# Optimization experiments

Hardware: AMD Instinct MI355X
Metric: run time of the kernel (lower is better)

The kernel has to match this reference:

```python
import jax, jax.numpy as jnp
import numpy as np

C = 0.11512925464970229  # ln(10)/20
K = 15
FD = 128
FS = 160
OV = 40
MAX_LAG = 256
PAD_L = K // 2
PAD_R = K - 1 - PAD_L
LOG_GAIN_LIMIT = 10 * C
GAIN_A = (6.0 * C - (-6.0 * C)) / 2
GAIN_B = (6.0 * C + (-6.0 * C)) / 2


def setup_inputs() -> dict:
    key = jax.random.key(0)
    ks = jax.random.split(key, 8)
    B, NF = 32, 500
    N = NF * FS
    x = jax.random.normal(ks[0], (B, 1, N), dtype=jnp.float32)
    features = jax.random.normal(ks[1], (B, NF, FD), dtype=jnp.float32)
    lags = jax.random.randint(ks[2], (B, NF), 0, 256)
    s = 1.0 / np.sqrt(FD)
    ck_w = jax.random.normal(ks[3], (K, FD), dtype=jnp.float32) * s
    ck_b = jax.random.normal(ks[4], (K,), dtype=jnp.float32) * 0.01
    fg_w = jax.random.normal(ks[5], (1, FD), dtype=jnp.float32) * s
    fg_b = jnp.full((1,), max(0.1, 4.0 + LOG_GAIN_LIMIT), dtype=jnp.float32)
    gg_w = jax.random.normal(ks[6], (1, FD), dtype=jnp.float32) * s
    gg_b = jax.random.normal(ks[7], (1,), dtype=jnp.float32) * 0.01
    return {"x": x, "features": features, "lags": lags,
            "ck_w": ck_w, "ck_b": ck_b, "fg_w": fg_w, "fg_b": fg_b,
            "gg_w": gg_w, "gg_b": gg_b}


def reference(x, features, lags, ck_w, ck_b, fg_w, fg_b, gg_w, gg_b):
    B, _, N = x.shape
    NF = features.shape[1]
    OUT = FS + OV  # per-frame output length before crossfade

    # per-frame FIR kernels, p=2 normalized over taps
    kernels = jnp.einsum('bfd,kd->bfk', features, ck_w) + ck_b          # (B,NF,K)
    kernels = kernels / (1e-6 + jnp.sqrt(jnp.sum(kernels**2, -1, keepdims=True)))
    # per-frame scalar gains
    gains = jnp.exp(-jax.nn.relu(features @ fg_w[0] + fg_b[0]) + LOG_GAIN_LIMIT)   # (B,NF)
    ggains = jnp.exp(GAIN_A * jnp.tanh(features @ gg_w[0] + gg_b[0]) + GAIN_B)     # (B,NF)

    # pad: [PAD_L,PAD_R] for conv, then [MAX_LAG, OV] for lag gather / final frame
    xp = jnp.pad(x[:, 0, :], ((0, 0), (MAX_LAG + PAD_L, PAD_R + OV)))   # (B,Np)

    L = FS + K - 1 + OV
    t = jnp.arange(L)
    f_off = jnp.arange(NF) * FS
    cidx = t[None, None, :] + f_off[None, :, None] + MAX_LAG - lags[:, :, None]  # (B,NF,L)
    xx = xp[jnp.arange(B)[:, None, None], cidx]                         # (B,NF,L)

    # grouped conv1d == cross-correlation with per-frame kernel
    win = jnp.stack([xx[:, :, k:k + OUT] for k in range(K)], axis=-1)   # (B,NF,OUT,K)
    conv = jnp.einsum('bflk,bfk->bfl', win, kernels)                    # (B,NF,OUT)

    # dry path
    offset = MAX_LAG + PAD_L
    pt_idx = offset + f_off[:, None] + jnp.arange(OUT)[None, :]         # (NF,OUT)
    pt = xp[:, pt_idx]                                                  # (B,NF,OUT)

    new_chunk = ggains[:, :, None] * (conv * gains[:, :, None] + pt)    # (B,NF,OUT)

    # overlap-add crossfade between consecutive frames
    win2 = 0.5 + 0.5 * jnp.cos((jnp.arange(OV) + 0.5) * jnp.pi / OV)
    win1 = win2[::-1]
    tails = new_chunk[:, :, FS:]                                        # (B,NF,OV)
    prev = jnp.concatenate([jnp.zeros_like(tails[:, :1]), tails[:, :-1]], axis=1)
    head = new_chunk[:, :, :OV] * win1 + prev * win2
    out = jnp.concatenate([head, new_chunk[:, :, OV:FS]], axis=-1)      # (B,NF,FS)
    return out.reshape(B, 1, NF * FS)
```

## Files before the change

kernel.cpp:

```cpp
#include <hip/hip_runtime.h>
#include <math.h>

namespace {
constexpr int K = 15;
constexpr int FD = 128;
constexpr int FS = 160;
constexpr int OV = 40;
constexpr int NFRAMES = 500;
constexpr int NSAMP = NFRAMES * FS;
constexpr float C_CONST = 0.11512925464970229f;
constexpr float LOG_GAIN_LIMIT = 10.0f * C_CONST;
constexpr float GAIN_A = 6.0f * C_CONST;
constexpr int FPB = 10;
constexpr int NFR = FPB + 1;
constexpr int WIN = FS + OV + K - 1;
constexpr int SFSTR = 132;
constexpr float PI_F = 3.14159265358979323846f;
}

__global__ __launch_bounds__(256)
void comb_fused(const float* __restrict__ x,
                const float* __restrict__ feat,
                const int*   __restrict__ lags,
                const float* __restrict__ ck_w,
                const float* __restrict__ ck_b,
                const float* __restrict__ fg_w,
                const float* __restrict__ fg_b,
                const float* __restrict__ gg_w,
                const float* __restrict__ gg_b,
                float* __restrict__ out)
{
    const int tid = threadIdx.x;
    const int bid = blockIdx.x;
    const int b   = bid / (NFRAMES / FPB);
    const int blk = bid - b * (NFRAMES / FPB);
    const int f0  = blk * FPB;

    __shared__ float sf[NFR][SFSTR];
    __shared__ float swin[NFR][WIN];
    __shared__ float sdots[NFR][17];
    __shared__ float sfk[NFR][16];
    __shared__ int   sbase[NFR];
    __shared__ int   svalid[NFR];

    const float* xb = x + (size_t)b * NSAMP;

    if (tid < NFR) {
        const int pf = f0 - 1 + tid;
        const int valid = (pf >= 0) ? 1 : 0;
        svalid[tid] = valid;
        sbase[tid]  = valid ? (pf * FS - lags[b * NFRAMES + pf] - 7) : 0;
    }
    for (int i = tid; i < NFR * (FD / 4); i += 256) {
        const int fr = i >> 5;
        const int e4 = i & 31;
        const int pf = f0 - 1 + fr;
        float4 v = make_float4(0.f, 0.f, 0.f, 0.f);
        if (pf >= 0)
            v = ((const float4*)feat)[((size_t)b * NFRAMES + pf) * (FD / 4) + e4];
        *(float4*)&sf[fr][e4 * 4] = v;
    }
    __syncthreads();

    for (int i = tid; i < NFR * WIN; i += 256) {
        const int fr = i / WIN;
        const int l  = i - fr * WIN;
        const int idx = sbase[fr] + l;
        float v = 0.f;
        if (svalid[fr] && idx >= 0 && idx < NSAMP) v = xb[idx];
        swin[fr][l] = v;
    }

    if (tid < NFR * 17) {
        const int fr = tid / 17;
        const int j  = tid - fr * 17;
        const float* wrow = (j < K) ? (ck_w + (size_t)j * FD)
                                    : ((j == K) ? fg_w : gg_w);
        const float4* w4 = (const float4*)wrow;
        const float4* f4 = (const float4*)&sf[fr][0];
        float4 acc = make_float4(0.f, 0.f, 0.f, 0.f);
        #pragma unroll
        for (int i = 0; i < FD / 4; ++i) {
            const float4 a = f4[i];
            const float4 w = w4[i];
            acc.x += a.x * w.x; acc.y += a.y * w.y;
            acc.z += a.z * w.z; acc.w += a.w * w.w;
        }
        const float bias = (j < K) ? ck_b[j] : ((j == K) ? fg_b[0] : gg_b[0]);
        sdots[fr][j] = acc.x + acc.y + acc.z + acc.w + bias;
    }
    __syncthreads();

    if (tid < NFR) {
        const int fr = tid;
        if (!svalid[fr]) {
            #pragma unroll
            for (int k = 0; k < 16; ++k) sfk[fr][k] = 0.f;
        } else {
            float kern[K];
            float n2 = 0.f;
            #pragma unroll
            for (int k = 0; k < K; ++k) {
                kern[k] = sdots[fr][k];
                n2 += kern[k] * kern[k];
            }
            const float inv   = 1.f / (1e-6f + sqrtf(n2));
            const float gain  = expf(-fmaxf(sdots[fr][K], 0.f) + LOG_GAIN_LIMIT);
            const float ggain = expf(GAIN_A * tanhf(sdots[fr][K + 1]));
            const float ks    = ggain * gain * inv;
            #pragma unroll
            for (int k = 0; k < K; ++k) sfk[fr][k] = ks * kern[k];
            sfk[fr][15] = ggain;
        }
    }
    __syncthreads();

    const int obase = f0 * FS;
    for (int o = tid; o < FPB * FS; o += 256) {
        const int frl = o / FS;
        const int t   = o - frl * FS;
        const int fr  = frl + 1;
        const float pt = xb[obase + o];
        float c = 0.f;
        #pragma unroll
        for (int k = 0; k < K; ++k)
            c += swin[fr][t + k] * sfk[fr][k];
        float val = c + sfk[fr][15] * pt;
        if (t < OV) {
            float ct = 0.f;
            #pragma unroll
            for (int k = 0; k < K; ++k)
                ct += swin[fr - 1][FS + t + k] * sfk[fr - 1][k];
            const float tail = ct + sfk[fr - 1][15] * pt;
            const float w2 = 0.5f + 0.5f * cosf(((float)t + 0.5f) * (PI_F / OV));
            val = val * (1.f - w2) + tail * w2;
        }
        out[(size_t)b * NSAMP + obase + o] = val;
    }
}

extern "C" void kernel_launch(void* const* d_in, const int* in_sizes, int n_in,
                              void* d_out, int out_size, void* d_ws, size_t ws_size,
                              hipStream_t stream) {
    const float* x    = (const float*)d_in[0];
    const float* feat = (const float*)d_in[1];
    const int*   lags = (const int*)d_in[2];
    const float* ck_w = (const float*)d_in[3];
    const float* ck_b = (const float*)d_in[4];
    const float* fg_w = (const float*)d_in[5];
    const float* fg_b = (const float*)d_in[6];
    const float* gg_w = (const float*)d_in[7];
    const float* gg_b = (const float*)d_in[8];
    float* out = (float*)d_out;

    const int B = in_sizes[0] / NSAMP;
    const int nblocks = B * (NFRAMES / FPB);
    comb_fused<<<dim3(nblocks), dim3(256), 0, stream>>>(
        x, feat, lags, ck_w, ck_b, fg_w, fg_b, gg_w, gg_b, out);
}
```

Measured before the change: 108.0 us.

## Vectorize window loads and compute four outputs per thread with register reuse

```diff
diff --git a/kernel.cpp b/kernel.cpp
--- a/kernel.cpp
+++ b/kernel.cpp
@@ -13,7 +13,8 @@
 constexpr float GAIN_A = 6.0f * C_CONST;
 constexpr int FPB = 10;
 constexpr int NFR = FPB + 1;
-constexpr int WIN = FS + OV + K - 1;
+constexpr int NW4 = 55;
+constexpr int WINA = 220;
 constexpr int SFSTR = 132;
 constexpr float PI_F = 3.14159265358979323846f;
 }
@@ -36,21 +37,14 @@
     const int blk = bid - b * (NFRAMES / FPB);
     const int f0  = blk * FPB;
 
-    __shared__ float sf[NFR][SFSTR];
-    __shared__ float swin[NFR][WIN];
+    __shared__ __align__(16) float sf[NFR][SFSTR];
+    __shared__ __align__(16) float swin[NFR][WINA];
     __shared__ float sdots[NFR][17];
-    __shared__ float sfk[NFR][16];
-    __shared__ int   sbase[NFR];
-    __shared__ int   svalid[NFR];
+    __shared__ __align__(16) float sfk[NFR][16];
+    __shared__ __align__(16) float swin2[OV + 8];
 
     const float* xb = x + (size_t)b * NSAMP;
 
-    if (tid < NFR) {
-        const int pf = f0 - 1 + tid;
-        const int valid = (pf >= 0) ? 1 : 0;
-        svalid[tid] = valid;
-        sbase[tid]  = valid ? (pf * FS - lags[b * NFRAMES + pf] - 7) : 0;
-    }
     for (int i = tid; i < NFR * (FD / 4); i += 256) {
         const int fr = i >> 5;
         const int e4 = i & 31;
@@ -60,16 +54,30 @@
             v = ((const float4*)feat)[((size_t)b * NFRAMES + pf) * (FD / 4) + e4];
         *(float4*)&sf[fr][e4 * 4] = v;
     }
+
+    for (int i = tid; i < NFR * NW4; i += 256) {
+        const int fr = i / NW4;
+        const int m  = i - fr * NW4;
+        const int pf = f0 - 1 + fr;
+        float4 v = make_float4(0.f, 0.f, 0.f, 0.f);
+        if (pf >= 0) {
+            const int base = pf * FS - lags[b * NFRAMES + pf] - 7;
+            const int idx  = base + 4 * m;
+            if (idx >= 0 && idx + 3 < NSAMP) {
+                v = *(const float4*)(xb + idx);
+            } else {
+                if (idx     >= 0 && idx     < NSAMP) v.x = xb[idx];
+                if (idx + 1 >= 0 && idx + 1 < NSAMP) v.y = xb[idx + 1];
+                if (idx + 2 >= 0 && idx + 2 < NSAMP) v.z = xb[idx + 2];
+                if (idx + 3 >= 0 && idx + 3 < NSAMP) v.w = xb[idx + 3];
+            }
+        }
+        *(float4*)&swin[fr][4 * m] = v;
+    }
+
+    if (tid < OV)
+        swin2[tid] = 0.5f + 0.5f * cosf(((float)tid + 0.5f) * (PI_F / OV));
     __syncthreads();
-
-    for (int i = tid; i < NFR * WIN; i += 256) {
-        const int fr = i / WIN;
-        const int l  = i - fr * WIN;
-        const int idx = sbase[fr] + l;
-        float v = 0.f;
-        if (svalid[fr] && idx >= 0 && idx < NSAMP) v = xb[idx];
-        swin[fr][l] = v;
-    }
 
     if (tid < NFR * 17) {
         const int fr = tid / 17;
@@ -92,50 +100,98 @@
     __syncthreads();
 
     if (tid < NFR) {
-        const int fr = tid;
-        if (!svalid[fr]) {
-            #pragma unroll
-            for (int k = 0; k < 16; ++k) sfk[fr][k] = 0.f;
+        const int pf = f0 - 1 + tid;
+        if (pf < 0) {
+            #pragma unroll
+            for (int k = 0; k < 16; ++k) sfk[tid][k] = 0.f;
         } else {
             float kern[K];
             float n2 = 0.f;
             #pragma unroll
             for (int k = 0; k < K; ++k) {
-                kern[k] = sdots[fr][k];
+                kern[k] = sdots[tid][k];
                 n2 += kern[k] * kern[k];
             }
             const float inv   = 1.f / (1e-6f + sqrtf(n2));
-            const float gain  = expf(-fmaxf(sdots[fr][K], 0.f) + LOG_GAIN_LIMIT);
-            const float ggain = expf(GAIN_A * tanhf(sdots[fr][K + 1]));
+            const float gain  = expf(-fmaxf(sdots[tid][K], 0.f) + LOG_GAIN_LIMIT);
+            const float ggain = expf(GAIN_A * tanhf(sdots[tid][K + 1]));
             const float ks    = ggain * gain * inv;
             #pragma unroll
-            for (int k = 0; k < K; ++k) sfk[fr][k] = ks * kern[k];
-            sfk[fr][15] = ggain;
+            for (int k = 0; k < K; ++k) sfk[tid][k] = ks * kern[k];
+            sfk[tid][15] = ggain;
         }
     }
     __syncthreads();
 
     const int obase = f0 * FS;
-    for (int o = tid; o < FPB * FS; o += 256) {
-        const int frl = o / FS;
-        const int t   = o - frl * FS;
+    for (int g = tid; g < FPB * (FS / 4); g += 256) {
+        const int frl = g / (FS / 4);
+        const int gi  = g - frl * (FS / 4);
+        const int t   = gi * 4;
         const int fr  = frl + 1;
-        const float pt = xb[obase + o];
-        float c = 0.f;
+
+        const float4 k0 = *(const float4*)&sfk[fr][0];
+        const float4 k1 = *(const float4*)&sfk[fr][4];
+        const float4 k2 = *(const float4*)&sfk[fr][8];
+        const float4 k3 = *(const float4*)&sfk[fr][12];
+        const float kc[16] = {k0.x,k0.y,k0.z,k0.w, k1.x,k1.y,k1.z,k1.w,
+                              k2.x,k2.y,k2.z,k2.w, k3.x,k3.y,k3.z,k3.w};
+
+        float w[20];
         #pragma unroll
-        for (int k = 0; k < K; ++k)
-            c += swin[fr][t + k] * sfk[fr][k];
-        float val = c + sfk[fr][15] * pt;
-        if (t < OV) {
-            float ct = 0.f;
-            #pragma unroll
-            for (int k = 0; k < K; ++k)
-                ct += swin[fr - 1][FS + t + k] * sfk[fr - 1][k];
-            const float tail = ct + sfk[fr - 1][15] * pt;
-            const float w2 = 0.5f + 0.5f * cosf(((float)t + 0.5f) * (PI_F / OV));
-            val = val * (1.f - w2) + tail * w2;
-        }
-        out[(size_t)b * NSAMP + obase + o] = val;
+        for (int q = 0; q < 5; ++q)
+            *(float4*)&w[4 * q] = *(const float4*)&swin[fr][t + 4 * q];
+
+        const float4 pt = *(const float4*)(xb + obase + frl * FS + t);
+
+        float4 res;
+        {
+            float c0 = 0.f, c1 = 0.f, c2 = 0.f, c3 = 0.f;
+            #pragma unroll
+            for (int k = 0; k < K; ++k) {
+                const float kk = kc[k];
+                c0 += w[k]     * kk;
+                c1 += w[k + 1] * kk;
+                c2 += w[k + 2] * kk;
+                c3 += w[k + 3] * kk;
+            }
+            const float ps = kc[15];
+            res.x = c0 + ps * pt.x; res.y = c1 + ps * pt.y;
+            res.z = c2 + ps * pt.z; res.w = c3 + ps * pt.w;
+        }
+
+        if (gi < OV / 4) {
+            const float4 q0 = *(const float4*)&sfk[fr - 1][0];
+            const float4 q1 = *(const float4*)&sfk[fr - 1][4];
+            const float4 q2 = *(const float4*)&sfk[fr - 1][8];
+            const float4 q3 = *(const float4*)&sfk[fr - 1][12];
+            const float qc[16] = {q0.x,q0.y,q0.z,q0.w, q1.x,q1.y,q1.z,q1.w,
+                                  q2.x,q2.y,q2.z,q2.w, q3.x,q3.y,q3.z,q3.w};
+            float wv[20];
+            #pragma unroll
+            for (int q = 0; q < 5; ++q)
+                *(float4*)&wv[4 * q] = *(const float4*)&swin[fr - 1][FS + t + 4 * q];
+
+            float c0 = 0.f, c1 = 0.f, c2 = 0.f, c3 = 0.f;
+            #pragma unroll
+            for (int k = 0; k < K; ++k) {
+                const float kk = qc[k];
+                c0 += wv[k]     * kk;
+                c1 += wv[k + 1] * kk;
+                c2 += wv[k + 2] * kk;
+                c3 += wv[k + 3] * kk;
+            }
+            const float ps = qc[15];
+            const float4 tail = make_float4(c0 + ps * pt.x, c1 + ps * pt.y,
+                                            c2 + ps * pt.z, c3 + ps * pt.w);
+            const float4 w2 = *(const float4*)&swin2[t];
+            res.x = res.x * (1.f - w2.x) + tail.x * w2.x;
+            res.y = res.y * (1.f - w2.y) + tail.y * w2.y;
+            res.z = res.z * (1.f - w2.z) + tail.z * w2.z;
+            res.w = res.w * (1.f - w2.w) + tail.w * w2.w;
+        }
+
+        *(float4*)(out + (size_t)b * NSAMP + obase + frl * FS + t) = res;
     }
 }
 
```

Measured after the change: 106.4 us. About the same (-1.5%).
